# Kernel tuning notes

Measured on AMD Instinct MI355X. Metric: run time of the kernel, lower is better.

## Reference

```python
import jax, jax.numpy as jnp
import numpy as np

N_NODES = 400
HID = 96
DEC = 64
FEAT_STATIC = 8
FEAT = FEAT_STATIC + N_NODES  # 408
EPS = 1e-8


def prelu(x, a):
    # single-parameter PReLU (torch default num_parameters=1)
    return jnp.where(x >= 0, x, a * x)


def setup_inputs() -> dict:
    key = jax.random.key(0)
    ks = jax.random.split(key, 16)
    B = 16
    E = N_NODES * (N_NODES - 1) // 2  # 79800

    x = jax.random.normal(ks[0], (B, E), dtype=jnp.float32)
    node_features = jax.random.normal(ks[1], (B, N_NODES, FEAT_STATIC), dtype=jnp.float32)
    sc_matrix = jax.random.uniform(ks[2], (B, N_NODES, N_NODES), dtype=jnp.float32)

    # normalization buffers (computed from train split in torch; random stand-ins)
    static_mean = jax.random.normal(ks[3], (1, 1, FEAT_STATIC), dtype=jnp.float32) * 0.1
    static_std = jnp.ones((1, 1, FEAT_STATIC), dtype=jnp.float32)

    def lin(k, fin, fout):
        kw, kb = jax.random.split(k)
        lim = 1.0 / np.sqrt(fin)
        W = jax.random.uniform(kw, (fin, fout), minval=-lim, maxval=lim, dtype=jnp.float32)
        b = jax.random.uniform(kb, (fout,), minval=-lim, maxval=lim, dtype=jnp.float32)
        return W, b

    W_e1, b_e1 = lin(ks[4], FEAT, HID)
    W_e2, b_e2 = lin(ks[5], HID, HID)
    W_d1, b_d1 = lin(ks[6], 3 * HID, DEC)  # symmetric decoder: 3 * node_embed_dim
    W_d2, b_d2 = lin(ks[7], DEC, DEC)
    W_d3, b_d3 = lin(ks[8], DEC, 1)

    a25 = jnp.float32(0.25)

    ei_np, ej_np = np.triu_indices(N_NODES, k=1)
    ei = jnp.asarray(ei_np, dtype=jnp.int32)
    ej = jnp.asarray(ej_np, dtype=jnp.int32)

    return {
        "x": x, "node_features": node_features, "sc_matrix": sc_matrix,
        "static_mean": static_mean, "static_std": static_std,
        "W_e1": W_e1, "b_e1": b_e1, "a_e1": a25,
        "W_e2": W_e2, "b_e2": b_e2, "a_e2": a25,
        "W_d1": W_d1, "b_d1": b_d1, "a_d1": a25,
        "W_d2": W_d2, "b_d2": b_d2, "a_d2": a25,
        "W_d3": W_d3, "b_d3": b_d3,
        "ei": ei, "ej": ej,
    }


def reference(x, node_features, sc_matrix, static_mean, static_std,
              W_e1, b_e1, a_e1, W_e2, b_e2, a_e2,
              W_d1, b_d1, a_d1, W_d2, b_d2, a_d2, W_d3, b_d3, ei, ej):
    # x (SC upper triangle) is only used for batch size in the torch module.
    # static anatomical block: z-score with train stats
    s = (node_features - static_mean) / (static_std + EPS)  # [B,N,8]
    # sc_row block, 'brain_scale': divide by per-matrix mean
    m = sc_matrix / jnp.maximum(
        jnp.mean(sc_matrix, axis=(-2, -1), keepdims=True), EPS)  # [B,N,N]
    feats = jnp.concatenate([s, m], axis=-1)  # [B,N,408]

    # shared node encoder (dropout inactive at eval)
    h = prelu(feats @ W_e1 + b_e1, a_e1)
    h = prelu(h @ W_e2 + b_e2, a_e2)  # [B,N,96]

    # per-edge gather over upper-triangle indices
    h_i = h[:, ei, :]  # [B,E,96]
    h_j = h[:, ej, :]
    # symmetric edge features
    edge_feat = jnp.concatenate(
        [h_i + h_j, jnp.abs(h_i - h_j), h_i * h_j], axis=-1)  # [B,E,288]

    z = prelu(edge_feat @ W_d1 + b_d1, a_d1)
    z = prelu(z @ W_d2 + b_d2, a_d2)
    out = (z @ W_d3 + b_d3)[..., 0]  # [B,E]
    return out
```

## Files before the change

### kernel.cpp

```cpp
#include <hip/hip_runtime.h>

#define NN 400
#define HID 96
#define EDGES 79800
#define BATCH 16
#define ROWS (BATCH*EDGES)
#define NT 13
#define NPAIRS 91

typedef _Float16 f16;
typedef f16 f16x2 __attribute__((ext_vector_type(2)));
typedef f16 f16x8 __attribute__((ext_vector_type(8)));
typedef __fp16 fp16x2 __attribute__((ext_vector_type(2)));
typedef float f32x16 __attribute__((ext_vector_type(16)));
typedef unsigned int u32;
typedef unsigned long long u64;

union H8 { f16x8 h; u32 u[4]; f16x2 p[4]; fp16x2 q[4]; u64 d[2]; };
union C2 { f16x2 h; fp16x2 q; u32 u; };

__device__ inline f16x2 pkrtz(float a, float b) {
  C2 c; c.q = __builtin_amdgcn_cvt_pkrtz(a, b); return c.h;
}
__device__ inline u32 pkrtz_u(float a, float b) {
  C2 c; c.q = __builtin_amdgcn_cvt_pkrtz(a, b); return c.u;
}
__device__ inline float fdot2a(f16x2 a, f16x2 b, float c) {
#if __has_builtin(__builtin_amdgcn_fdot2)
  C2 ca, cb; ca.h = a; cb.h = b;
  return __builtin_amdgcn_fdot2(ca.q, cb.q, c, false);
#else
  return c + (float)a.x*(float)b.x + (float)a.y*(float)b.y;
#endif
}

__device__ inline f16x8 habs8(f16x8 x) {
  H8 t; t.h = x;
  t.u[0] &= 0x7fff7fffu; t.u[1] &= 0x7fff7fffu;
  t.u[2] &= 0x7fff7fffu; t.u[3] &= 0x7fff7fffu;
  return t.h;
}

__device__ inline f16x8 pack8(float a0,float a1,float a2,float a3,
                              float a4,float a5,float a6,float a7){
  H8 u;
  u.p[0] = pkrtz(a0,a1);
  u.p[1] = pkrtz(a2,a3);
  u.p[2] = pkrtz(a4,a5);
  u.p[3] = pkrtz(a6,a7);
  return u.h;
}

__device__ inline void plswap(u32 &x, u32 &y) {
  auto r = __builtin_amdgcn_permlane32_swap((int)x, (int)y, false, false);
  x = (u32)r[0]; y = (u32)r[1];
}

#define MEMFENCE asm volatile("" ::: "memory")

__global__ void prep_mean_kernel(const float* __restrict__ We1, const float* __restrict__ We2,
                                 const float* __restrict__ W1, const float* __restrict__ W2,
                                 const float* __restrict__ sc,
                                 u32* __restrict__ wq, float* __restrict__ mpart) {
  if (blockIdx.x >= 140) {
    int p = blockIdx.x - 140;
    int b = p >> 4, part = p & 15;
    const float4* src = (const float4*)(sc + (size_t)b*160000) + part*2500;
    float s = 0.f;
    for (int i = threadIdx.x; i < 2500; i += 256) {
      float4 v = src[i];
      s += (v.x + v.y) + (v.z + v.w);
    }
    __shared__ float red[256];
    red[threadIdx.x] = s; __syncthreads();
    for (int off = 128; off > 0; off >>= 1) {
      if (threadIdx.x < off) red[threadIdx.x] += red[threadIdx.x + off];
      __syncthreads();
    }
    if (threadIdx.x == 0) mpart[p] = red[0];
    return;
  }
  int D = blockIdx.x*256 + threadIdx.x;
  float v0, v1;
  if (D < 9216) {
    int frag = D >> 8;  int t = frag >> 1, q = frag & 1;
    int rem = D & 255;  int lane = rem >> 2, dj = rem & 3;
    int c = lane & 31, h2 = lane >> 5;
    int k = 16*t + 8*h2 + 2*dj;
    int d = 32*q + c;
    v0 = W1[k*64 + d]; v1 = W1[(k+1)*64 + d];
  } else if (D < 11264) {
    int Dl = D - 9216;
    int frag = Dl >> 8; int t2 = frag >> 1, q = frag & 1;
    int rem = Dl & 255; int lane = rem >> 2, dj = rem & 3;
    int c = lane & 31, h2 = lane >> 5;
    int k = 16*t2 + 8*h2 + 2*dj;
    int d = 32*q + c;
    v0 = W2[k*64 + d]; v1 = W2[(k+1)*64 + d];
  } else if (D < 31232) {
    int Dl = D - 11264;
    int frag = Dl >> 8; int t = frag/3, ct = frag - 3*t;
    int rem = Dl & 255; int lane = rem >> 2, dj = rem & 3;
    int c = lane & 31, h2 = lane >> 5;
    int k0 = 16*t + 8*h2 + 2*dj, k1 = k0 + 1;
    int d = 32*ct + c;
    v0 = (k0 < 400) ? We1[(8+k0)*96 + d] : (k0 < 408 ? We1[(k0-400)*96 + d] : 0.f);
    v1 = (k1 < 400) ? We1[(8+k1)*96 + d] : (k1 < 408 ? We1[(k1-400)*96 + d] : 0.f);
  } else {
    int Dl = D - 31232;
    int frag = Dl >> 8; int t = frag/3, ct = frag - 3*t;
    int rem = Dl & 255; int lane = rem >> 2, dj = rem & 3;
    int c = lane & 31, h2 = lane >> 5;
    int k = 16*t + 8*h2 + 2*dj;
    int d = 32*ct + c;
    v0 = We2[k*96 + d]; v1 = We2[(k+1)*96 + d];
  }
  wq[D] = pkrtz_u(v0, v1);
}

__global__ __launch_bounds__(256) void enc_kernel(
    const float* __restrict__ sc, const float* __restrict__ nf,
    const float* __restrict__ smean, const float* __restrict__ sstd,
    const float* __restrict__ be1, const float* __restrict__ ae1,
    const float* __restrict__ be2, const float* __restrict__ ae2,
    const float* __restrict__ mpart, const u32* __restrict__ wq,
    f16* __restrict__ hout) {
  __shared__ u32 lds[12288 + 1664];
  const int tid = threadIdx.x;
  const int wid = tid >> 6, lane = tid & 63;
  const int c = lane & 31, h2 = lane >> 5;
  const int r0 = blockIdx.x * 32;
  {
    int row = tid >> 3, seg = tid & 7;
    int r = r0 + row;
    int b = r / 400;
    float ms = 0.f;
    const float4* mp4 = (const float4*)(mpart + 16*b);
#pragma unroll
    for (int k = 0; k < 4; ++k) { float4 v = mp4[k]; ms += (v.x+v.y)+(v.z+v.w); }
    float rm = 1.f / fmaxf(ms*(1.f/160000.f), 1e-8f);
    const float4* src = (const float4*)(sc + (size_t)r*400);
#pragma unroll
    for (int i = 0; i < 13; ++i) {
      int col4 = seg + 8*i;
      if (col4 < 100) {
        float4 v = src[col4];
        u32 lo = pkrtz_u(v.x*rm, v.y*rm);
        u32 hi = pkrtz_u(v.z*rm, v.w*rm);
        *(u64*)(lds + row*210 + col4*2) = (u64)lo | ((u64)hi << 32);
      }
    }
  }
  __syncthreads();
  int tb = (wid==0) ? 0 : (wid==1) ? 7 : (wid==2) ? 14 : 20;
  int te = (wid==0) ? 7 : (wid==1) ? 14 : (wid==2) ? 20 : 26;
  f32x16 acc[3] = {};
  const u32* wb1 = wq + 11264;
  for (int t = tb; t < te; ++t) {
    f16x8 af;
    if (t < 25) {
      H8 av;
      const u32* ap = lds + c*210 + 8*t + 4*h2;
      av.d[0] = *(const u64*)ap;
      av.d[1] = *(const u64*)(ap + 2);
      af = av.h;
    } else {
      af = (f16x8){};
      if (h2 == 0) {
        int r = r0 + c;
        float q0[8];
#pragma unroll
        for (int j = 0; j < 8; ++j)
          q0[j] = (nf[r*8 + j] - smean[j]) / (sstd[j] + 1e-8f);
        af = pack8(q0[0],q0[1],q0[2],q0[3],q0[4],q0[5],q0[6],q0[7]);
      }
    }
#pragma unroll
    for (int ct = 0; ct < 3; ++ct) {
      f16x8 bf = *(const f16x8*)(wb1 + ((t*3+ct)*64 + lane)*4);
      acc[ct] = __builtin_amdgcn_mfma_f32_32x32x16_f16(af, bf, acc[ct], 0,0,0);
    }
  }
  __syncthreads();
#pragma unroll
  for (int ct = 0; ct < 3; ++ct) {
    union { f32x16 v; float4 f[4]; } u; u.v = acc[ct];
#pragma unroll
    for (int i4 = 0; i4 < 4; ++i4)
      *(float4*)(lds + (((wid*3+ct)*4 + i4)*64 + lane)*4) = u.f[i4];
  }
  __syncthreads();
  f16* zb16 = (f16*)(lds + 12288);
  const float a1 = *ae1;
  if (wid < 3) {
    float bv = be1[32*wid + c];
    f32x16 s;
#pragma unroll
    for (int i = 0; i < 16; ++i) s[i] = bv;
#pragma unroll
    for (int w2 = 0; w2 < 4; ++w2) {
#pragma unroll
      for (int i4 = 0; i4 < 4; ++i4) {
        float4 f = *(const float4*)(lds + (((w2*3+wid)*4 + i4)*64 + lane)*4);
        s[4*i4+0] += f.x; s[4*i4+1] += f.y; s[4*i4+2] += f.z; s[4*i4+3] += f.w;
      }
    }
#pragma unroll
    for (int r = 0; r < 16; ++r) {
      float v = s[r]; v = fmaxf(v, a1*v);
      int row = (r & 3) + 8*(r >> 2) + 4*h2;
      zb16[row*104 + 32*wid + c] = (f16)v;
    }
  }
  __syncthreads();
  if (wid < 3) {
    const float a2 = *ae2;
    float bv = be2[32*wid + c];
    f32x16 acc2;
#pragma unroll
    for (int i = 0; i < 16; ++i) acc2[i] = bv;
    const u32* wb2 = wq + 31232;
#pragma unroll
    for (int t = 0; t < 6; ++t) {
      f16x8 af = *(const f16x8*)(zb16 + c*104 + 16*t + 8*h2);
      f16x8 bf = *(const f16x8*)(wb2 + ((t*3+wid)*64 + lane)*4);
      acc2 = __builtin_amdgcn_mfma_f32_32x32x16_f16(af, bf, acc2, 0,0,0);
    }
#pragma unroll
    for (int rr = 0; rr < 16; ++rr) {
      int row = (rr & 3) + 8*(rr >> 2) + 4*h2;
      float v = acc2[rr]; v = fmaxf(v, a2*v);
      hout[(r0 + row)*96 + 32*wid + c] = (f16)v;
    }
  }
}

__global__ __launch_bounds__(256, 2) void decoder_kernel(
    const f16* __restrict__ hbuf, const u32* __restrict__ wq,
    const float* __restrict__ b1, const float* __restrict__ b2,
    const float* __restrict__ ad1, const float* __restrict__ ad2,
    const float* __restrict__ W3, const float* __restrict__ b3p,
    float* __restrict__ out) {
  __shared__ alignas(16) u32 smem[12800];
  const int tid = threadIdx.x;
  int p = blockIdx.x;
  int b = p / NPAIRS, pr = p - b*NPAIRS;
  int I = 0;
  while (pr >= NT - I) { pr -= NT - I; ++I; }
  const int J = I + pr;
  for (int i = tid; i < 384; i += 256) {
    int row = i / 12, off = i - row*12;
    int nb = I*32 + row; nb = nb < NN ? nb : NN-1;
    const float4* src = (const float4*)(hbuf + (size_t)(b*NN + nb)*HID) + off;
    *((float4*)(smem + row*48) + off) = *src;
  }
  {
    float4* dst = (float4*)(smem + 1536);
    const float4* srcw = (const float4*)wq;
    for (int i = tid; i < 2816; i += 256) dst[i] = srcw[i];
  }

  const int lane = tid & 63;
  const int wid  = tid >> 6;
  const int c = lane & 31, h2 = lane >> 5;
  const int gj = J*32 + c;
  const int gjc = gj < NN ? gj : NN-1;
  f16x8 hjr[6];
  {
    const f16* hjp = hbuf + (size_t)(b*NN + gjc)*HID + 8*h2;
#pragma unroll
    for (int t = 0; t < 6; ++t) hjr[t] = *(const f16x8*)(hjp + 16*t);
  }
  const float a1 = *ad1, a2 = *ad2, b3 = *b3p;
  const f16x2 a1v = pkrtz(a1, a1);
  const f16x2 a2v = pkrtz(a2, a2);
  f16x8 bcst = (f16x8){};
  f16x8 ab1f[2]; ab1f[0] = (f16x8){}; ab1f[1] = (f16x8){};
  f16x8 ab2f[2]; ab2f[0] = (f16x8){}; ab2f[1] = (f16x8){};
  if (h2 == 0) {
    bcst[0] = (f16)1.f;
    ab1f[0][0] = (f16)b1[c];      ab1f[1][0] = (f16)b1[32 + c];
    ab2f[0][0] = (f16)b2[c];      ab2f[1][0] = (f16)b2[32 + c];
  }
  f16x2 w3q[2][8];
#pragma unroll
  for (int q2 = 0; q2 < 2; ++q2)
#pragma unroll
    for (int a = 0; a < 8; ++a) {
      int base = 32*q2 + 8*(a >> 1) + 2*(a & 1) + 4*h2;
      w3q[q2][a] = pkrtz(W3[base], W3[base + 1]);
    }
  __syncthreads();

  const f16* hIb = (const f16*)smem;
  const u32* wfr = smem + 1536;
  const u32* w2a = smem + 10752;
  const int bofs = b*EDGES;

#define LDW(n, tt) \
  n##s0 = *(const f16x8*)(wfr + ((((tt)    )*2+0)*64 + lane)*4); \
  n##s1 = *(const f16x8*)(wfr + ((((tt)    )*2+1)*64 + lane)*4); \
  n##d0 = *(const f16x8*)(wfr + ((((tt)+ 6)*2+0)*64 + lane)*4); \
  n##d1 = *(const f16x8*)(wfr + ((((tt)+ 6)*2+1)*64 + lane)*4); \
  n##p0 = *(const f16x8*)(wfr + ((((tt)+12)*2+0)*64 + lane)*4); \
  n##p1 = *(const f16x8*)(wfr + ((((tt)+12)*2+1)*64 + lane)*4); \
  n##h0 = *(const f16x8*)(hi0 + 16*(tt) + 8*h2); \
  n##h1 = *(const f16x8*)(hi1 + 16*(tt) + 8*h2)

#define STEP(n, tt) { \
  f16x8 hj8 = hjr[tt]; \
  f16x8 su0 = n##h0 + hj8, di0 = habs8(n##h0 - hj8), pr0 = n##h0 * hj8; \
  f16x8 su1 = n##h1 + hj8, di1 = habs8(n##h1 - hj8), pr1 = n##h1 * hj8; \
  __builtin_amdgcn_s_setprio(1); \
  acc[0][0] = __builtin_amdgcn_mfma_f32_32x32x16_f16(n##s0, su0, acc[0][0],0,0,0); \
  acc[0][1] = __builtin_amdgcn_mfma_f32_32x32x16_f16(n##s1, su0, acc[0][1],0,0,0); \
  acc[1][0] = __builtin_amdgcn_mfma_f32_32x32x16_f16(n##s0, su1, acc[1][0],0,0,0); \
  acc[1][1] = __builtin_amdgcn_mfma_f32_32x32x16_f16(n##s1, su1, acc[1][1],0,0,0); \
  acc[0][0] = __builtin_amdgcn_mfma_f32_32x32x16_f16(n##d0, di0, acc[0][0],0,0,0); \
  acc[0][1] = __builtin_amdgcn_mfma_f32_32x32x16_f16(n##d1, di0, acc[0][1],0,0,0); \
  acc[1][0] = __builtin_amdgcn_mfma_f32_32x32x16_f16(n##d0, di1, acc[1][0],0,0,0); \
  acc[1][1] = __builtin_amdgcn_mfma_f32_32x32x16_f16(n##d1, di1, acc[1][1],0,0,0); \
  acc[0][0] = __builtin_amdgcn_mfma_f32_32x32x16_f16(n##p0, pr0, acc[0][0],0,0,0); \
  acc[0][1] = __builtin_amdgcn_mfma_f32_32x32x16_f16(n##p1, pr0, acc[0][1],0,0,0); \
  acc[1][0] = __builtin_amdgcn_mfma_f32_32x32x16_f16(n##p0, pr1, acc[1][0],0,0,0); \
  acc[1][1] = __builtin_amdgcn_mfma_f32_32x32x16_f16(n##p1, pr1, acc[1][1],0,0,0); \
  __builtin_amdgcn_s_setprio(0); }

#pragma unroll 1
  for (int it = 0; it < 4; ++it) {
    MEMFENCE;
    const int i0 = it*8 + wid*2;
    const f16* hi0 = hIb + (i0+0)*HID;
    const f16* hi1 = hIb + (i0+1)*HID;
    f32x16 acc[2][2] = {};
    acc[0][0] = __builtin_amdgcn_mfma_f32_32x32x16_f16(ab1f[0], bcst, acc[0][0], 0,0,0);
    acc[0][1] = __builtin_amdgcn_mfma_f32_32x32x16_f16(ab1f[1], bcst, acc[0][1], 0,0,0);
    acc[1][0] = __builtin_amdgcn_mfma_f32_32x32x16_f16(ab1f[0], bcst, acc[1][0], 0,0,0);
    acc[1][1] = __builtin_amdgcn_mfma_f32_32x32x16_f16(ab1f[1], bcst, acc[1][1], 0,0,0);
    f16x8 As0,As1,Ad0,Ad1,Ap0,Ap1,Ah0,Ah1;
    f16x8 Bs0,Bs1,Bd0,Bd1,Bp0,Bp1,Bh0,Bh1;
    LDW(A, 0); MEMFENCE;
    LDW(B, 1); MEMFENCE; STEP(A, 0);
    LDW(A, 2); MEMFENCE; STEP(B, 1);
    LDW(B, 3); MEMFENCE; STEP(A, 2);
    LDW(A, 4); MEMFENCE; STEP(B, 3);
    LDW(B, 5); MEMFENCE; STEP(A, 4);
    STEP(B, 5);
    MEMFENCE;
    f16x8 w2r[4][2];
#pragma unroll
    for (int t2 = 0; t2 < 4; ++t2) {
      w2r[t2][0] = *(const f16x8*)(w2a + ((t2*2+0)*64 + lane)*4);
      w2r[t2][1] = *(const f16x8*)(w2a + ((t2*2+1)*64 + lane)*4);
    }
    MEMFENCE;
#pragma unroll
    for (int m = 0; m < 2; ++m) {
      u32 w[16];
#pragma unroll
      for (int q = 0; q < 2; ++q)
#pragma unroll
        for (int a = 0; a < 8; ++a) {
          f16x2 pz = pkrtz(acc[m][q][2*a], acc[m][q][2*a+1]);
          pz = __builtin_elementwise_max(pz, pz * a1v);
          C2 cv; cv.h = pz; w[q*8 + a] = cv.u;
        }
#pragma unroll
      for (int g = 0; g < 4; ++g) {
        plswap(w[g*4+0], w[g*4+2]);
        plswap(w[g*4+1], w[g*4+3]);
      }
      f32x16 zacc[2] = {};
      zacc[0] = __builtin_amdgcn_mfma_f32_32x32x16_f16(ab2f[0], bcst, zacc[0], 0,0,0);
      zacc[1] = __builtin_amdgcn_mfma_f32_32x32x16_f16(ab2f[1], bcst, zacc[1], 0,0,0);
      __builtin_amdgcn_s_setprio(1);
#pragma unroll
      for (int t2 = 0; t2 < 4; ++t2) {
        H8 zf; zf.u[0] = w[4*t2]; zf.u[1] = w[4*t2+1]; zf.u[2] = w[4*t2+2]; zf.u[3] = w[4*t2+3];
        zacc[0] = __builtin_amdgcn_mfma_f32_32x32x16_f16(w2r[t2][0], zf.h, zacc[0], 0,0,0);
        zacc[1] = __builtin_amdgcn_mfma_f32_32x32x16_f16(w2r[t2][1], zf.h, zacc[1], 0,0,0);
      }
      __builtin_amdgcn_s_setprio(0);
      float s0 = 0.f, s1 = 0.f;
#pragma unroll
      for (int a = 0; a < 8; ++a) {
        f16x2 pz0 = pkrtz(zacc[0][2*a], zacc[0][2*a+1]);
        pz0 = __builtin_elementwise_max(pz0, pz0 * a2v);
        s0 = fdot2a(pz0, w3q[0][a], s0);
        f16x2 pz1 = pkrtz(zacc[1][2*a], zacc[1][2*a+1]);
        pz1 = __builtin_elementwise_max(pz1, pz1 * a2v);
        s1 = fdot2a(pz1, w3q[1][a], s1);
      }
      float ssum = s0 + s1;
      ssum += __shfl_xor(ssum, 32);
      int gi = I*32 + i0 + m;
      if (h2 == 0 && gi < gj && gj < NN) {
        int eo = bofs + gi*(799 - gi)/2 + (gj - gi - 1);
        out[eo] = ssum + b3;
      }
    }
  }
#undef LDW
#undef STEP
}

extern "C" void kernel_launch(void* const* d_in, const int* in_sizes, int n_in,
                              void* d_out, int out_size, void* d_ws, size_t ws_size,
                              hipStream_t stream) {
  const float* nf  = (const float*)d_in[1];
  const float* sc  = (const float*)d_in[2];
  const float* sm  = (const float*)d_in[3];
  const float* ss  = (const float*)d_in[4];
  const float* We1 = (const float*)d_in[5];
  const float* be1 = (const float*)d_in[6];
  const float* ae1 = (const float*)d_in[7];
  const float* We2 = (const float*)d_in[8];
  const float* be2 = (const float*)d_in[9];
  const float* ae2 = (const float*)d_in[10];
  const float* W1  = (const float*)d_in[11];
  const float* b1  = (const float*)d_in[12];
  const float* a1  = (const float*)d_in[13];
  const float* W2  = (const float*)d_in[14];
  const float* b2  = (const float*)d_in[15];
  const float* a2  = (const float*)d_in[16];
  const float* W3  = (const float*)d_in[17];
  const float* b3  = (const float*)d_in[18];
  float* out = (float*)d_out;

  char* ws = (char*)d_ws;
  float* mpart = (float*)ws;
  f16*   hbuf = (f16*)(ws + 1024);
  u32*   wq   = (u32*)(ws + 1024 + 1228800);

  prep_mean_kernel<<<396, 256, 0, stream>>>(We1, We2, W1, W2, sc, wq, mpart);
  enc_kernel<<<200, 256, 0, stream>>>(sc, nf, sm, ss, be1, ae1, be2, ae2,
                                      mpart, wq, hbuf);
  decoder_kernel<<<BATCH*NPAIRS, 256, 0, stream>>>(hbuf, wq, b1, b2, a1, a2,
                                                   W3, b3, out);
}
```

Baseline: 183.3 us.

## Restructure encoder layer-1 to per-wave column tiles with register-prefetched weights

The encoder's first GEMM used to split the K dimension across four waves and then reduce the partial sums through LDS. Now three waves each own one 32-column output tile over the full K range, so the LDS reduction and its extra barriers go away. All layer-1 and layer-2 weight fragments plus the static-feature fragment are loaded into registers before the first barrier, overlapping those global loads with the LDS staging. This lowers LDS use, but one wave sits idle during compute and register pressure rises by about 128 VGPRs for the weights.

```diff
diff --git a/kernel.cpp b/kernel.cpp
--- a/kernel.cpp
+++ b/kernel.cpp
@@ -125,7 +125,7 @@
     const float* __restrict__ be2, const float* __restrict__ ae2,
     const float* __restrict__ mpart, const u32* __restrict__ wq,
     f16* __restrict__ hout) {
-  __shared__ u32 lds[12288 + 1664];
+  __shared__ u32 lds[6720 + 1600];
   const int tid = threadIdx.x;
   const int wid = tid >> 6, lane = tid & 63;
   const int c = lane & 31, h2 = lane >> 5;
@@ -151,65 +151,48 @@
       }
     }
   }
+  f16x8 bfr[26], we2r[6], af25;
+  if (wid < 3) {
+    const u32* wb1 = wq + 11264;
+#pragma unroll
+    for (int t = 0; t < 26; ++t)
+      bfr[t] = *(const f16x8*)(wb1 + ((t*3+wid)*64 + lane)*4);
+    const u32* wb2 = wq + 31232;
+#pragma unroll
+    for (int t = 0; t < 6; ++t)
+      we2r[t] = *(const f16x8*)(wb2 + ((t*3+wid)*64 + lane)*4);
+    af25 = (f16x8){};
+    if (h2 == 0) {
+      int r = r0 + c;
+      float q0[8];
+#pragma unroll
+      for (int j = 0; j < 8; ++j)
+        q0[j] = (nf[r*8 + j] - smean[j]) / (sstd[j] + 1e-8f);
+      af25 = pack8(q0[0],q0[1],q0[2],q0[3],q0[4],q0[5],q0[6],q0[7]);
+    }
+  }
   __syncthreads();
-  int tb = (wid==0) ? 0 : (wid==1) ? 7 : (wid==2) ? 14 : 20;
-  int te = (wid==0) ? 7 : (wid==1) ? 14 : (wid==2) ? 20 : 26;
-  f32x16 acc[3] = {};
-  const u32* wb1 = wq + 11264;
-  for (int t = tb; t < te; ++t) {
-    f16x8 af;
-    if (t < 25) {
+  f16* zb16 = (f16*)(lds + 6720);
+  if (wid < 3) {
+    const float a1 = *ae1;
+    float bv = be1[32*wid + c];
+    f32x16 acc;
+#pragma unroll
+    for (int i = 0; i < 16; ++i) acc[i] = bv;
+#pragma unroll
+    for (int t = 0; t < 25; ++t) {
       H8 av;
       const u32* ap = lds + c*210 + 8*t + 4*h2;
       av.d[0] = *(const u64*)ap;
       av.d[1] = *(const u64*)(ap + 2);
-      af = av.h;
-    } else {
-      af = (f16x8){};
-      if (h2 == 0) {
-        int r = r0 + c;
-        float q0[8];
-#pragma unroll
-        for (int j = 0; j < 8; ++j)
-          q0[j] = (nf[r*8 + j] - smean[j]) / (sstd[j] + 1e-8f);
-        af = pack8(q0[0],q0[1],q0[2],q0[3],q0[4],q0[5],q0[6],q0[7]);
-      }
-    }
-#pragma unroll
-    for (int ct = 0; ct < 3; ++ct) {
-      f16x8 bf = *(const f16x8*)(wb1 + ((t*3+ct)*64 + lane)*4);
-      acc[ct] = __builtin_amdgcn_mfma_f32_32x32x16_f16(af, bf, acc[ct], 0,0,0);
-    }
-  }
-  __syncthreads();
-#pragma unroll
-  for (int ct = 0; ct < 3; ++ct) {
-    union { f32x16 v; float4 f[4]; } u; u.v = acc[ct];
-#pragma unroll
-    for (int i4 = 0; i4 < 4; ++i4)
-      *(float4*)(lds + (((wid*3+ct)*4 + i4)*64 + lane)*4) = u.f[i4];
-  }
-  __syncthreads();
-  f16* zb16 = (f16*)(lds + 12288);
-  const float a1 = *ae1;
-  if (wid < 3) {
-    float bv = be1[32*wid + c];
-    f32x16 s;
-#pragma unroll
-    for (int i = 0; i < 16; ++i) s[i] = bv;
-#pragma unroll
-    for (int w2 = 0; w2 < 4; ++w2) {
-#pragma unroll
-      for (int i4 = 0; i4 < 4; ++i4) {
-        float4 f = *(const float4*)(lds + (((w2*3+wid)*4 + i4)*64 + lane)*4);
-        s[4*i4+0] += f.x; s[4*i4+1] += f.y; s[4*i4+2] += f.z; s[4*i4+3] += f.w;
-      }
-    }
+      acc = __builtin_amdgcn_mfma_f32_32x32x16_f16(av.h, bfr[t], acc, 0,0,0);
+    }
+    acc = __builtin_amdgcn_mfma_f32_32x32x16_f16(af25, bfr[25], acc, 0,0,0);
 #pragma unroll
     for (int r = 0; r < 16; ++r) {
-      float v = s[r]; v = fmaxf(v, a1*v);
+      float v = acc[r]; v = fmaxf(v, a1*v);
       int row = (r & 3) + 8*(r >> 2) + 4*h2;
-      zb16[row*104 + 32*wid + c] = (f16)v;
+      zb16[row*100 + 32*wid + c] = (f16)v;
     }
   }
   __syncthreads();
@@ -219,12 +202,10 @@
     f32x16 acc2;
 #pragma unroll
     for (int i = 0; i < 16; ++i) acc2[i] = bv;
-    const u32* wb2 = wq + 31232;
 #pragma unroll
     for (int t = 0; t < 6; ++t) {
-      f16x8 af = *(const f16x8*)(zb16 + c*104 + 16*t + 8*h2);
-      f16x8 bf = *(const f16x8*)(wb2 + ((t*3+wid)*64 + lane)*4);
-      acc2 = __builtin_amdgcn_mfma_f32_32x32x16_f16(af, bf, acc2, 0,0,0);
+      f16x8 af = *(const f16x8*)(zb16 + c*100 + 16*t + 8*h2);
+      acc2 = __builtin_amdgcn_mfma_f32_32x32x16_f16(af, we2r[t], acc2, 0,0,0);
     }
 #pragma unroll
     for (int rr = 0; rr < 16; ++rr) {
```

Measured after the change: 178.8 us. 1.02x faster.
